# Kernel tuning notes

Hardware: AMD Instinct MI355X
Metric: run time of the kernel (lower is better)

Reference implementation:

```python
import jax, jax.numpy as jnp
import numpy as np

D_MODEL = 1024
N_HEADS = 16
HEAD_DIM = D_MODEL // N_HEADS
BATCH = 2
SEQ = 2048
MASK_FILL = -10000.0


def setup_inputs() -> dict:
    key = jax.random.key(0)
    ks = jax.random.split(key, 5)
    scale = 1.0 / np.sqrt(D_MODEL)
    return {
        "x": jax.random.normal(ks[0], (BATCH, SEQ, D_MODEL), dtype=jnp.float32),
        "w_q": jax.random.normal(ks[1], (D_MODEL, D_MODEL), dtype=jnp.float32) * scale,
        "w_k": jax.random.normal(ks[2], (D_MODEL, D_MODEL), dtype=jnp.float32) * scale,
        "w_v": jax.random.normal(ks[3], (D_MODEL, D_MODEL), dtype=jnp.float32) * scale,
        "w_o": jax.random.normal(ks[4], (D_MODEL, D_MODEL), dtype=jnp.float32) * scale,
    }


def reference(x, w_q, w_k, w_v, w_o):
    B, S, C = x.shape
    # Linear(bias=False): y = x @ W^T (torch stores W as [out, in])
    q = jnp.einsum("bsc,dc->bsd", x, w_q).reshape(B, S, N_HEADS, HEAD_DIM)
    k = jnp.einsum("bsc,dc->bsd", x, w_k).reshape(B, S, N_HEADS, HEAD_DIM)
    v = jnp.einsum("bsc,dc->bsd", x, w_v).reshape(B, S, N_HEADS, HEAD_DIM)
    # scores: [B, H, S, S]
    scores = jnp.einsum("bqhd,bkhd->bhqk", q, k) / np.sqrt(HEAD_DIM)
    causal = jnp.tril(jnp.ones((S, S), dtype=bool))
    scores = jnp.where(causal, scores, MASK_FILL)
    weights = jax.nn.softmax(scores, axis=-1)
    out = jnp.einsum("bhqk,bkhd->bqhd", weights, v).reshape(B, S, C)
    return jnp.einsum("bsc,dc->bsd", out, w_o)
```

## Files before the change

kernel.cpp:

```cpp
#include <hip/hip_runtime.h>

typedef __attribute__((ext_vector_type(8))) short bf16x8;
typedef __attribute__((ext_vector_type(4))) float floatx4;

static constexpr int SEQ    = 2048;
static constexpr int CDIM   = 1024;
static constexpr int NH     = 16;
static constexpr int HD     = 64;
static constexpr int NBATCH = 2;
static constexpr int MROWS  = NBATCH * SEQ;

static __device__ __forceinline__ short f2bf(float f) {
    union { float f; unsigned u; } x; x.f = f;
    unsigned r = x.u + 0x7fffu + ((x.u >> 16) & 1u);
    return (short)(r >> 16);
}

static __device__ __forceinline__ unsigned pack2bf(float lo, float hi) {
    return ((unsigned)(unsigned short)f2bf(hi) << 16) | (unsigned)(unsigned short)f2bf(lo);
}

static __device__ __forceinline__ unsigned pk2(float lo, float hi) {
    union { float f; unsigned u; } a, b; a.f = lo; b.f = hi;
    return __builtin_amdgcn_perm(b.u + 0x8000u, a.u + 0x8000u, 0x07060302u);
}

static __device__ __forceinline__ floatx4 mfma16(bf16x8 a, bf16x8 b, floatx4 c) {
    return __builtin_amdgcn_mfma_f32_16x16x32_bf16(a, b, c, 0, 0, 0);
}

static __device__ __forceinline__ void gl_lds16(const short* g, short* l) {
    __builtin_amdgcn_global_load_lds(
        (const __attribute__((address_space(1))) void*)g,
        (__attribute__((address_space(3))) void*)l, 16, 0, 0);
}

__global__ void convert_all(
    const void* __restrict__ x,  const void* __restrict__ wq,
    const void* __restrict__ wk, const void* __restrict__ wv,
    const void* __restrict__ wo,
    short* __restrict__ xc,  short* __restrict__ wqc, short* __restrict__ wkc,
    short* __restrict__ wvc, short* __restrict__ woc,
    int* __restrict__ flag)
{
    const int tid = threadIdx.x;
    const unsigned short* xs = (const unsigned short*)x;
    int pl = 0;
    for (int i = tid; i < 2048; i += 256) {
        const int e = (xs[2 * i] >> 7) & 0xFF;
        if (e >= 110 && e <= 144) pl++;
    }
    #pragma unroll
    for (int off = 32; off > 0; off >>= 1) pl += __shfl_down(pl, off, 64);
    __shared__ int cnt;
    if (tid == 0) cnt = 0;
    __syncthreads();
    if ((tid & 63) == 0) atomicAdd(&cnt, pl);
    __syncthreads();
    const int f = (cnt < 1024) ? 1 : 0;
    if (blockIdx.x == 0 && blockIdx.y == 0 && tid == 0) *flag = f;

    const int y = blockIdx.y;
    const void* src = (y == 0) ? x  : (y == 1) ? wq : (y == 2) ? wk : (y == 3) ? wv : wo;
    short*      dst = (y == 0) ? xc : (y == 1) ? wqc : (y == 2) ? wkc : (y == 3) ? wvc : woc;
    const int n4 = (y == 0) ? (MROWS * CDIM / 4) : (CDIM * CDIM / 4);

    const int stride = gridDim.x * blockDim.x;
    for (int i = blockIdx.x * blockDim.x + tid; i < n4; i += stride) {
        if (f) {
            const float4 v = ((const float4*)src)[i];
            ((uint2*)dst)[i] = make_uint2(pack2bf(v.x, v.y), pack2bf(v.z, v.w));
        } else {
            ((uint2*)dst)[i] = ((const uint2*)src)[i];
        }
    }
}

__global__ __launch_bounds__(256) void gemm_bt128(
    const short* __restrict__ A,
    const short* __restrict__ W0, const short* __restrict__ W1, const short* __restrict__ W2,
    void* __restrict__ C0, void* __restrict__ C1, void* __restrict__ C2,
    short* __restrict__ VT, const int* __restrict__ flag)
{
    const int m0  = blockIdx.x * 128;
    const int sel = blockIdx.y >> 3;
    const int n0  = (blockIdx.y & 7) * 128;
    const short* W = (sel == 0) ? W0 : ((sel == 1) ? W1 : W2);
    void*        C = (sel == 0) ? C0 : ((sel == 1) ? C1 : C2);
    const bool f32out = (flag != nullptr) && (*flag != 0);
    const bool vtout  = (sel == 2) && (VT != nullptr);

    __shared__ __align__(16) short ta[128 * 64];
    __shared__ __align__(16) short tb[128 * 64];

    const int tid  = threadIdx.x;
    const int lane = tid & 63;
    const int wave = tid >> 6;
    const int quad = lane >> 4;
    const int l16  = lane & 15;
    const int wm   = (wave >> 1) * 64;
    const int wn   = (wave & 1) * 64;

    floatx4 acc[4][4];
    #pragma unroll
    for (int i = 0; i < 4; i++)
        #pragma unroll
        for (int j = 0; j < 4; j++)
            acc[i][j] = 0.0f;

    const int sr8 = lane >> 3;
    const int ug  = ((lane & 7) ^ sr8) * 8;
    const short* Ab = A + (size_t)(m0 + 32 * wave + sr8) * CDIM + ug;
    const short* Wb = W + (size_t)(n0 + 32 * wave + sr8) * CDIM + ug;
    short* ta0 = ta + (32 * wave) * 64;
    short* tb0 = tb + (32 * wave) * 64;

    for (int k0 = 0; k0 < CDIM; k0 += 64) {
        __syncthreads();
        gl_lds16(Ab + k0,             ta0);
        gl_lds16(Ab +  8 * CDIM + k0, ta0 +  8 * 64);
        gl_lds16(Ab + 16 * CDIM + k0, ta0 + 16 * 64);
        gl_lds16(Ab + 24 * CDIM + k0, ta0 + 24 * 64);
        gl_lds16(Wb + k0,             tb0);
        gl_lds16(Wb +  8 * CDIM + k0, tb0 +  8 * 64);
        gl_lds16(Wb + 16 * CDIM + k0, tb0 + 16 * 64);
        gl_lds16(Wb + 24 * CDIM + k0, tb0 + 24 * 64);
        __syncthreads();

        #pragma unroll
        for (int kc = 0; kc < 2; kc++) {
            const int pu = (((kc * 4 + quad) ^ (l16 & 7))) * 8;
            bf16x8 af[4], bw[4];
            #pragma unroll
            for (int i = 0; i < 4; i++)
                af[i] = *(const bf16x8*)(ta + (wm + i * 16 + l16) * 64 + pu);
            #pragma unroll
            for (int j = 0; j < 4; j++)
                bw[j] = *(const bf16x8*)(tb + (wn + j * 16 + l16) * 64 + pu);
            #pragma unroll
            for (int i = 0; i < 4; i++)
                #pragma unroll
                for (int j = 0; j < 4; j++)
                    acc[i][j] = mfma16(af[i], bw[j], acc[i][j]);
        }
    }

    #pragma unroll
    for (int i = 0; i < 4; i++) {
        #pragma unroll
        for (int j = 0; j < 4; j++) {
            const int row0 = m0 + wm + i * 16 + quad * 4;
            const int col  = n0 + wn + j * 16 + l16;
            if (vtout) {
                const int bb  = row0 >> 11;
                const int key = row0 & 2047;
                const size_t idx = ((size_t)(bb * 1024 + col)) * 2048 + key;
                *(uint2*)(VT + idx) = make_uint2(pk2(acc[i][j][0], acc[i][j][1]),
                                                 pk2(acc[i][j][2], acc[i][j][3]));
            } else if (f32out) {
                float* cp = (float*)C + (size_t)row0 * CDIM + col;
                #pragma unroll
                for (int r = 0; r < 4; r++)
                    cp[(size_t)r * CDIM] = acc[i][j][r];
            } else {
                short* cp = (short*)C + (size_t)row0 * CDIM + col;
                #pragma unroll
                for (int r = 0; r < 4; r++)
                    cp[(size_t)r * CDIM] = f2bf(acc[i][j][r]);
            }
        }
    }
}

__global__ __launch_bounds__(256, 2) void attn_t(
    const short* __restrict__ Q, const short* __restrict__ K,
    const short* __restrict__ VT, short* __restrict__ O)
{
    const int h = blockIdx.x;
    const int b = blockIdx.y;
    const int z  = blockIdx.z;
    const int qt2 = (z < 8) ? (15 - z) : (z - 8);
    const int nkt = qt2 + 1;

    const int tid  = threadIdx.x;
    const int lane = tid & 63;
    const int wave = tid >> 6;
    const int quad = lane >> 4;
    const int l16  = lane & 15;

    __shared__ __align__(16) short Kt[128][72];
    __shared__ __align__(16) short Vt[64][136];
    __shared__ __align__(16) short Pl[4][2][16][136];

    const int rowBase = b * SEQ;
    const int colH    = h * HD;
    const int qgA     = qt2 * 128 + wave * 16 + l16;
    const int qgB     = qgA + 64;

    bf16x8 qa0, qa1, qc0, qc1;
    {
        const short* qp = Q + (size_t)(rowBase + qgA) * CDIM + colH + quad * 8;
        qa0 = *(const bf16x8*)qp;
        qa1 = *(const bf16x8*)(qp + 32);
        const short* qp2 = qp + (size_t)64 * CDIM;
        qc0 = *(const bf16x8*)qp2;
        qc1 = *(const bf16x8*)(qp2 + 32);
    }

    floatx4 oA[4], oB[4];
    #pragma unroll
    for (int nd = 0; nd < 4; nd++) { oA[nd] = 0.0f; oB[nd] = 0.0f; }
    float lA = 0.0f, lB = 0.0f;

    const int kk = tid >> 1;
    const int kd = (tid & 1) * 32;
    const short* kg = K + (size_t)(rowBase + kk) * CDIM + colH + kd;
    const int sd = tid >> 2;
    const int sk = (tid & 3) * 32;
    const short* vg = VT + ((size_t)(b * NH + h) * HD + sd) * SEQ + sk;

    uint4 ka_0 = *(const uint4*)(kg);
    uint4 ka_1 = *(const uint4*)(kg + 8);
    uint4 ka_2 = *(const uint4*)(kg + 16);
    uint4 ka_3 = *(const uint4*)(kg + 24);
    uint4 va_0 = *(const uint4*)(vg);
    uint4 va_1 = *(const uint4*)(vg + 8);
    uint4 va_2 = *(const uint4*)(vg + 16);
    uint4 va_3 = *(const uint4*)(vg + 24);

    for (int kt = 0; kt < nkt; kt++) {
        __syncthreads();
        *(uint4*)&Kt[kk][kd]      = ka_0;
        *(uint4*)&Kt[kk][kd + 8]  = ka_1;
        *(uint4*)&Kt[kk][kd + 16] = ka_2;
        *(uint4*)&Kt[kk][kd + 24] = ka_3;
        *(uint4*)&Vt[sd][sk]      = va_0;
        *(uint4*)&Vt[sd][sk + 8]  = va_1;
        *(uint4*)&Vt[sd][sk + 16] = va_2;
        *(uint4*)&Vt[sd][sk + 24] = va_3;
        __syncthreads();

        if (kt + 1 < nkt) {
            const short* kn = kg + (size_t)(kt + 1) * 128 * CDIM;
            const short* vn = vg + (kt + 1) * 128;
            ka_0 = *(const uint4*)(kn);
            ka_1 = *(const uint4*)(kn + 8);
            ka_2 = *(const uint4*)(kn + 16);
            ka_3 = *(const uint4*)(kn + 24);
            va_0 = *(const uint4*)(vn);
            va_1 = *(const uint4*)(vn + 8);
            va_2 = *(const uint4*)(vn + 16);
            va_3 = *(const uint4*)(vn + 24);
        }

        const int key0 = kt * 128;
        const bool masked = (kt == nkt - 1);

        #pragma unroll
        for (int ms = 0; ms < 8; ms++) {
            const short* kp = &Kt[ms * 16 + l16][quad * 8];
            bf16x8 k0 = *(const bf16x8*)kp;
            bf16x8 k1 = *(const bf16x8*)(kp + 32);
            floatx4 sA = {0.f, 0.f, 0.f, 0.f};
            floatx4 sB = {0.f, 0.f, 0.f, 0.f};
            sA = mfma16(k0, qa0, sA);
            sB = mfma16(k0, qc0, sB);
            sA = mfma16(k1, qa1, sA);
            sB = mfma16(k1, qc1, sB);
            float pA[4], pB[4];
            #pragma unroll
            for (int r = 0; r < 4; r++) {
                const int kgl = key0 + ms * 16 + quad * 4 + r;
                float eA = __expf(sA[r] * 0.125f);
                float eB = __expf(sB[r] * 0.125f);
                if (masked) {
                    if (kgl > qgA) eA = 0.0f;
                    if (kgl > qgB) eB = 0.0f;
                }
                pA[r] = eA; lA += eA;
                pB[r] = eB; lB += eB;
            }
            *(uint2*)&Pl[wave][0][l16][ms * 16 + quad * 4] =
                make_uint2(pk2(pA[0], pA[1]), pk2(pA[2], pA[3]));
            *(uint2*)&Pl[wave][1][l16][ms * 16 + quad * 4] =
                make_uint2(pk2(pB[0], pB[1]), pk2(pB[2], pB[3]));
        }

        #pragma unroll
        for (int kc = 0; kc < 4; kc++) {
            const bf16x8 pbA = *(const bf16x8*)&Pl[wave][0][l16][kc * 32 + quad * 8];
            const bf16x8 pbB = *(const bf16x8*)&Pl[wave][1][l16][kc * 32 + quad * 8];
            #pragma unroll
            for (int nd = 0; nd < 4; nd++) {
                const bf16x8 va = *(const bf16x8*)&Vt[nd * 16 + l16][kc * 32 + quad * 8];
                oA[nd] = mfma16(va, pbA, oA[nd]);
                oB[nd] = mfma16(va, pbB, oB[nd]);
            }
        }
    }

    lA += __shfl_xor(lA, 16, 64);
    lA += __shfl_xor(lA, 32, 64);
    lB += __shfl_xor(lB, 16, 64);
    lB += __shfl_xor(lB, 32, 64);
    const float invA = 1.0f / lA;
    const float invB = 1.0f / lB;

    short* opA = O + (size_t)(rowBase + qgA) * CDIM + colH;
    short* opB = O + (size_t)(rowBase + qgB) * CDIM + colH;
    #pragma unroll
    for (int nd = 0; nd < 4; nd++) {
        *(uint2*)(opA + nd * 16 + quad * 4) =
            make_uint2(pk2(oA[nd][0] * invA, oA[nd][1] * invA),
                       pk2(oA[nd][2] * invA, oA[nd][3] * invA));
        *(uint2*)(opB + nd * 16 + quad * 4) =
            make_uint2(pk2(oB[nd][0] * invB, oB[nd][1] * invB),
                       pk2(oB[nd][2] * invB, oB[nd][3] * invB));
    }
}

extern "C" void kernel_launch(void* const* d_in, const int* in_sizes, int n_in,
                              void* d_out, int out_size, void* d_ws, size_t ws_size,
                              hipStream_t stream)
{
    const void* x  = d_in[0];
    const void* wq = d_in[1];
    const void* wk = d_in[2];
    const void* wv = d_in[3];
    const void* wo = d_in[4];

    int* flag = (int*)d_ws;
    short* w = (short*)((char*)d_ws + 256);
    const int ME  = 1024 * 1024;
    short* Wqc = w;
    short* Wkc = w + 1 * ME;
    short* Wvc = w + 2 * ME;
    short* Woc = w + 3 * ME;
    short* Xc  = w + 4 * ME;
    short* Qb  = w + 8 * ME;
    short* Kb  = w + 12 * ME;
    short* VTb = w + 16 * ME;
    short* Ob  = Xc;

    dim3 blk(256);
    convert_all<<<dim3(512, 5), blk, 0, stream>>>(
        x, wq, wk, wv, wo, Xc, Wqc, Wkc, Wvc, Woc, flag);

    gemm_bt128<<<dim3(MROWS / 128, 24), blk, 0, stream>>>(
        Xc, Wqc, Wkc, Wvc, Qb, Kb, nullptr, VTb, nullptr);
    attn_t<<<dim3(NH, NBATCH, SEQ / 128), blk, 0, stream>>>(Qb, Kb, VTb, Ob);
    gemm_bt128<<<dim3(MROWS / 128, 8), blk, 0, stream>>>(
        Ob, Woc, Woc, Woc, d_out, d_out, d_out, nullptr, flag);
}
```

Baseline: 182.3 us.

## Split attention keys across two blocks with combine kernel; add narrower output GEMM

```diff
diff --git a/kernel.cpp b/kernel.cpp
--- a/kernel.cpp
+++ b/kernel.cpp
@@ -23,6 +23,12 @@
 static __device__ __forceinline__ unsigned pk2(float lo, float hi) {
     union { float f; unsigned u; } a, b; a.f = lo; b.f = hi;
     return __builtin_amdgcn_perm(b.u + 0x8000u, a.u + 0x8000u, 0x07060302u);
+}
+
+static __device__ __forceinline__ float bf2f(short s) {
+    union { unsigned u; float f; } x;
+    x.u = ((unsigned)(unsigned short)s) << 16;
+    return x.f;
 }
 
 static __device__ __forceinline__ floatx4 mfma16(bf16x8 a, bf16x8 b, floatx4 c) {
@@ -172,15 +178,101 @@
     }
 }
 
+__global__ __launch_bounds__(256) void gemm_n64(
+    const short* __restrict__ A, const short* __restrict__ W,
+    void* __restrict__ C, const int* __restrict__ flag)
+{
+    const int m0 = blockIdx.x * 128;
+    const int n0 = blockIdx.y * 64;
+    const bool f32out = (flag != nullptr) && (*flag != 0);
+
+    __shared__ __align__(16) short ta[128 * 64];
+    __shared__ __align__(16) short tb[64 * 64];
+
+    const int tid  = threadIdx.x;
+    const int lane = tid & 63;
+    const int wave = tid >> 6;
+    const int quad = lane >> 4;
+    const int l16  = lane & 15;
+    const int wm   = (wave >> 1) * 64;
+    const int wn   = (wave & 1) * 32;
+
+    floatx4 acc[4][2];
+    #pragma unroll
+    for (int i = 0; i < 4; i++)
+        #pragma unroll
+        for (int j = 0; j < 2; j++)
+            acc[i][j] = 0.0f;
+
+    const int sr8 = lane >> 3;
+    const int ug  = ((lane & 7) ^ sr8) * 8;
+    const short* Ab = A + (size_t)(m0 + 32 * wave + sr8) * CDIM + ug;
+    const short* Wb = W + (size_t)(n0 + 16 * wave + sr8) * CDIM + ug;
+    short* ta0 = ta + (32 * wave) * 64;
+    short* tb0 = tb + (16 * wave) * 64;
+
+    for (int k0 = 0; k0 < CDIM; k0 += 64) {
+        __syncthreads();
+        gl_lds16(Ab + k0,             ta0);
+        gl_lds16(Ab +  8 * CDIM + k0, ta0 +  8 * 64);
+        gl_lds16(Ab + 16 * CDIM + k0, ta0 + 16 * 64);
+        gl_lds16(Ab + 24 * CDIM + k0, ta0 + 24 * 64);
+        gl_lds16(Wb + k0,             tb0);
+        gl_lds16(Wb +  8 * CDIM + k0, tb0 +  8 * 64);
+        __syncthreads();
+
+        #pragma unroll
+        for (int kc = 0; kc < 2; kc++) {
+            const int pu = (((kc * 4 + quad) ^ (l16 & 7))) * 8;
+            bf16x8 af[4], bw[2];
+            #pragma unroll
+            for (int i = 0; i < 4; i++)
+                af[i] = *(const bf16x8*)(ta + (wm + i * 16 + l16) * 64 + pu);
+            #pragma unroll
+            for (int j = 0; j < 2; j++)
+                bw[j] = *(const bf16x8*)(tb + (wn + j * 16 + l16) * 64 + pu);
+            #pragma unroll
+            for (int i = 0; i < 4; i++)
+                #pragma unroll
+                for (int j = 0; j < 2; j++)
+                    acc[i][j] = mfma16(af[i], bw[j], acc[i][j]);
+        }
+    }
+
+    #pragma unroll
+    for (int i = 0; i < 4; i++) {
+        #pragma unroll
+        for (int j = 0; j < 2; j++) {
+            const int row0 = m0 + wm + i * 16 + quad * 4;
+            const int col  = n0 + wn + j * 16 + l16;
+            if (f32out) {
+                float* cp = (float*)C + (size_t)row0 * CDIM + col;
+                #pragma unroll
+                for (int r = 0; r < 4; r++)
+                    cp[(size_t)r * CDIM] = acc[i][j][r];
+            } else {
+                short* cp = (short*)C + (size_t)row0 * CDIM + col;
+                #pragma unroll
+                for (int r = 0; r < 4; r++)
+                    cp[(size_t)r * CDIM] = f2bf(acc[i][j][r]);
+            }
+        }
+    }
+}
+
 __global__ __launch_bounds__(256, 2) void attn_t(
     const short* __restrict__ Q, const short* __restrict__ K,
-    const short* __restrict__ VT, short* __restrict__ O)
+    const short* __restrict__ VT,
+    short* __restrict__ P0, short* __restrict__ P1, float* __restrict__ L)
 {
     const int h = blockIdx.x;
     const int b = blockIdx.y;
-    const int z  = blockIdx.z;
-    const int qt2 = (z < 8) ? (15 - z) : (z - 8);
-    const int nkt = qt2 + 1;
+    const int z = blockIdx.z;
+    const int g = z >> 3;
+    const int item = (g == 1) ? (23 - z) : (g == 3) ? (55 - z) : z;
+    const int qt2 = 15 - (item >> 1);
+    const int p   = item & 1;
+    const int nktall = qt2 + 1;
 
     const int tid  = threadIdx.x;
     const int lane = tid & 63;
@@ -219,16 +311,18 @@
     const int sk = (tid & 3) * 32;
     const short* vg = VT + ((size_t)(b * NH + h) * HD + sd) * SEQ + sk;
 
-    uint4 ka_0 = *(const uint4*)(kg);
-    uint4 ka_1 = *(const uint4*)(kg + 8);
-    uint4 ka_2 = *(const uint4*)(kg + 16);
-    uint4 ka_3 = *(const uint4*)(kg + 24);
-    uint4 va_0 = *(const uint4*)(vg);
-    uint4 va_1 = *(const uint4*)(vg + 8);
-    uint4 va_2 = *(const uint4*)(vg + 16);
-    uint4 va_3 = *(const uint4*)(vg + 24);
-
-    for (int kt = 0; kt < nkt; kt++) {
+    const short* kg0 = kg + (size_t)p * 128 * CDIM;
+    const short* vg0 = vg + p * 128;
+    uint4 ka_0 = *(const uint4*)(kg0);
+    uint4 ka_1 = *(const uint4*)(kg0 + 8);
+    uint4 ka_2 = *(const uint4*)(kg0 + 16);
+    uint4 ka_3 = *(const uint4*)(kg0 + 24);
+    uint4 va_0 = *(const uint4*)(vg0);
+    uint4 va_1 = *(const uint4*)(vg0 + 8);
+    uint4 va_2 = *(const uint4*)(vg0 + 16);
+    uint4 va_3 = *(const uint4*)(vg0 + 24);
+
+    for (int kt = p; kt < nktall; kt += 2) {
         __syncthreads();
         *(uint4*)&Kt[kk][kd]      = ka_0;
         *(uint4*)&Kt[kk][kd + 8]  = ka_1;
@@ -240,9 +334,9 @@
         *(uint4*)&Vt[sd][sk + 24] = va_3;
         __syncthreads();
 
-        if (kt + 1 < nkt) {
-            const short* kn = kg + (size_t)(kt + 1) * 128 * CDIM;
-            const short* vn = vg + (kt + 1) * 128;
+        if (kt + 2 < nktall) {
+            const short* kn = kg + (size_t)(kt + 2) * 128 * CDIM;
+            const short* vn = vg + (kt + 2) * 128;
             ka_0 = *(const uint4*)(kn);
             ka_1 = *(const uint4*)(kn + 8);
             ka_2 = *(const uint4*)(kn + 16);
@@ -254,7 +348,7 @@
         }
 
         const int key0 = kt * 128;
-        const bool masked = (kt == nkt - 1);
+        const bool masked = (kt == nktall - 1);
 
         #pragma unroll
         for (int ms = 0; ms < 8; ms++) {
@@ -303,20 +397,46 @@
     lA += __shfl_xor(lA, 32, 64);
     lB += __shfl_xor(lB, 16, 64);
     lB += __shfl_xor(lB, 32, 64);
-    const float invA = 1.0f / lA;
-    const float invB = 1.0f / lB;
-
-    short* opA = O + (size_t)(rowBase + qgA) * CDIM + colH;
-    short* opB = O + (size_t)(rowBase + qgB) * CDIM + colH;
+
+    short* Pp = p ? P1 : P0;
+    float* Lp = L + p * (NBATCH * NH * SEQ);
+    short* opA = Pp + (size_t)(rowBase + qgA) * CDIM + colH;
+    short* opB = Pp + (size_t)(rowBase + qgB) * CDIM + colH;
     #pragma unroll
     for (int nd = 0; nd < 4; nd++) {
         *(uint2*)(opA + nd * 16 + quad * 4) =
-            make_uint2(pk2(oA[nd][0] * invA, oA[nd][1] * invA),
-                       pk2(oA[nd][2] * invA, oA[nd][3] * invA));
+            make_uint2(pk2(oA[nd][0], oA[nd][1]), pk2(oA[nd][2], oA[nd][3]));
         *(uint2*)(opB + nd * 16 + quad * 4) =
-            make_uint2(pk2(oB[nd][0] * invB, oB[nd][1] * invB),
-                       pk2(oB[nd][2] * invB, oB[nd][3] * invB));
-    }
+            make_uint2(pk2(oB[nd][0], oB[nd][1]), pk2(oB[nd][2], oB[nd][3]));
+    }
+    if (quad == 0) {
+        Lp[(b * NH + h) * SEQ + qgA] = lA;
+        Lp[(b * NH + h) * SEQ + qgB] = lB;
+    }
+}
+
+__global__ void combine(const short* __restrict__ P0, const short* __restrict__ P1,
+                        const float* __restrict__ L, short* __restrict__ Ob)
+{
+    const int i = blockIdx.x * blockDim.x + threadIdx.x;
+    const int row = i >> 7;
+    const int c8  = i & 127;
+    const int h   = c8 >> 3;
+    const int b   = row >> 11;
+    const int q   = row & 2047;
+    const int li  = (b * NH + h) * SEQ + q;
+    const float inv = 1.0f / (L[li] + L[NBATCH * NH * SEQ + li]);
+
+    const bf16x8 a0 = ((const bf16x8*)P0)[i];
+    const bf16x8 a1 = ((const bf16x8*)P1)[i];
+    unsigned d[4];
+    #pragma unroll
+    for (int e = 0; e < 4; e++) {
+        const float lo = (bf2f(a0[2 * e])     + bf2f(a1[2 * e]))     * inv;
+        const float hi = (bf2f(a0[2 * e + 1]) + bf2f(a1[2 * e + 1])) * inv;
+        d[e] = pk2(lo, hi);
+    }
+    ((uint4*)Ob)[i] = make_uint4(d[0], d[1], d[2], d[3]);
 }
 
 extern "C" void kernel_launch(void* const* d_in, const int* in_sizes, int n_in,
@@ -340,6 +460,9 @@
     short* Qb  = w + 8 * ME;
     short* Kb  = w + 12 * ME;
     short* VTb = w + 16 * ME;
+    short* P1b = w + 20 * ME;
+    float* Lb  = (float*)(w + 24 * ME);
+    short* P0b = Xc;
     short* Ob  = Xc;
 
     dim3 blk(256);
@@ -348,7 +471,8 @@
 
     gemm_bt128<<<dim3(MROWS / 128, 24), blk, 0, stream>>>(
         Xc, Wqc, Wkc, Wvc, Qb, Kb, nullptr, VTb, nullptr);
-    attn_t<<<dim3(NH, NBATCH, SEQ / 128), blk, 0, stream>>>(Qb, Kb, VTb, Ob);
-    gemm_bt128<<<dim3(MROWS / 128, 8), blk, 0, stream>>>(
-        Ob, Woc, Woc, Woc, d_out, d_out, d_out, nullptr, flag);
-}
+    attn_t<<<dim3(NH, NBATCH, 32), blk, 0, stream>>>(Qb, Kb, VTb, P0b, P1b, Lb);
+    combine<<<dim3(MROWS * CDIM / 8 / 256), blk, 0, stream>>>(P0b, P1b, Lb, Ob);
+    gemm_n64<<<dim3(MROWS / 128, CDIM / 64), blk, 0, stream>>>(
+        Ob, Woc, d_out, flag);
+}
```

After: 180.3 us. Within noise of the previous version (-1.1%).
